# Performance work log

Measured on AMD Instinct MI355X. Metric: run time of the kernel, lower is better.

Reference implementation:

```python
import jax, jax.numpy as jnp
import numpy as np

D_MODEL = 1024
N_HEAD = 16
D_HEAD = D_MODEL // N_HEAD
D_FF = 4096
EPS = 1e-5


def _layernorm(x, gamma, beta):
    mu = jnp.mean(x, axis=-1, keepdims=True)
    var = jnp.mean(jnp.square(x - mu), axis=-1, keepdims=True)
    return (x - mu) * jax.lax.rsqrt(var + EPS) * gamma + beta


def setup_inputs() -> dict:
    key = jax.random.key(0)
    ks = jax.random.split(key, 16)
    s = 1.0 / np.sqrt(D_MODEL)
    sf = 1.0 / np.sqrt(D_FF)
    return {
        "src": jax.random.normal(ks[0], (8, 1024, D_MODEL), dtype=jnp.float32),
        "Wq": jax.random.uniform(ks[1], (D_MODEL, D_MODEL), jnp.float32, -s, s),
        "bq": jnp.zeros((D_MODEL,), jnp.float32),
        "Wk": jax.random.uniform(ks[2], (D_MODEL, D_MODEL), jnp.float32, -s, s),
        "bk": jnp.zeros((D_MODEL,), jnp.float32),
        "Wv": jax.random.uniform(ks[3], (D_MODEL, D_MODEL), jnp.float32, -s, s),
        "bv": jnp.zeros((D_MODEL,), jnp.float32),
        "Wo": jax.random.uniform(ks[4], (D_MODEL, D_MODEL), jnp.float32, -s, s),
        "bo": jnp.zeros((D_MODEL,), jnp.float32),
        "W1": jax.random.uniform(ks[5], (D_MODEL, D_FF), jnp.float32, -s, s),
        "b1": jnp.zeros((D_FF,), jnp.float32),
        "W2": jax.random.uniform(ks[6], (D_FF, D_MODEL), jnp.float32, -sf, sf),
        "b2": jnp.zeros((D_MODEL,), jnp.float32),
        "g1": jnp.ones((D_MODEL,), jnp.float32),
        "beta1": jnp.zeros((D_MODEL,), jnp.float32),
        "g2": jnp.ones((D_MODEL,), jnp.float32),
        "beta2": jnp.zeros((D_MODEL,), jnp.float32),
    }


def reference(src, Wq, bq, Wk, bk, Wv, bv, Wo, bo, W1, b1, W2, b2, g1, beta1, g2, beta2):
    B, S, _ = src.shape
    x = _layernorm(src, g1, beta1)
    # QKV projections -> [B, H, S, Dh]
    def split_heads(t):
        return t.reshape(B, S, N_HEAD, D_HEAD).transpose(0, 2, 1, 3)
    q = split_heads(x @ Wq + bq)
    k = split_heads(x @ Wk + bk)
    v = split_heads(x @ Wv + bv)
    # SymbolicAttention (canonical graph): softmax(q k^T / sqrt(d_head)) v
    scores = jnp.einsum('bhqd,bhkd->bhqk', q, k) / np.sqrt(D_HEAD).astype(np.float32)
    attn = jax.nn.softmax(scores, axis=-1)
    ctx = jnp.einsum('bhqk,bhkd->bhqd', attn, v)
    ctx = ctx.transpose(0, 2, 1, 3).reshape(B, S, D_MODEL)
    src = src + (ctx @ Wo + bo)  # dropout is identity in eval
    y = _layernorm(src, g2, beta2)
    ffn = jax.nn.relu(y @ W1 + b1) @ W2 + b2
    return src + ffn
```

## Files before the change

### kernel.cpp

```cpp
#include <hip/hip_runtime.h>
#include <stdint.h>

#define D_MODEL 1024
#define N_HEAD  16
#define D_HEAD  64
#define D_FF    4096
#define SEQ     1024
#define BATCH   8
#define M_TOK   (BATCH*SEQ)

typedef __attribute__((ext_vector_type(8))) short bf16x8;
typedef __attribute__((ext_vector_type(4))) float f32x4;

__device__ __forceinline__ float bf2f(unsigned short u) {
    union { unsigned int u; float f; } x; x.u = ((unsigned int)u) << 16; return x.f;
}
__device__ __forceinline__ unsigned short f2bf(float f) {
    union { float f; unsigned int u; } x; x.f = f;
    unsigned int r = x.u + 0x7fffu + ((x.u >> 16) & 1u);
    return (unsigned short)(r >> 16);
}

typedef const __attribute__((address_space(1))) unsigned int* gas_t;
typedef __attribute__((address_space(3))) unsigned int* las_t;
__device__ __forceinline__ void gl_lds16(const unsigned short* g, unsigned short* l) {
    __builtin_amdgcn_global_load_lds((gas_t)g, (las_t)l, 16, 0, 0);
}

__global__ __launch_bounds__(256) void transpose_cvt(
        const float* __restrict__ src, unsigned short* __restrict__ dst,
        int R, int C)
{
    __shared__ float t[32][33];
    const int tx = threadIdx.x & 31, ty = threadIdx.x >> 5;
    const int c0 = blockIdx.x * 32, r0 = blockIdx.y * 32;
    #pragma unroll
    for (int i = 0; i < 32; i += 8)
        t[ty + i][tx] = src[(size_t)(r0 + ty + i) * C + c0 + tx];
    __syncthreads();
    #pragma unroll
    for (int i = 0; i < 32; i += 8)
        dst[(size_t)(c0 + ty + i) * R + r0 + tx] = f2bf(t[tx][ty + i]);
}

__global__ __launch_bounds__(256) void ln_kernel(
        const float* __restrict__ x, const float* __restrict__ g,
        const float* __restrict__ be, unsigned short* __restrict__ out)
{
    const int row = blockIdx.x, tid = threadIdx.x;
    const f32x4 v = *(const f32x4*)(x + (size_t)row * D_MODEL + tid * 4);
    float s  = v[0] + v[1] + v[2] + v[3];
    float ss = v[0]*v[0] + v[1]*v[1] + v[2]*v[2] + v[3]*v[3];
    #pragma unroll
    for (int o = 1; o < 64; o <<= 1) { s += __shfl_xor(s, o); ss += __shfl_xor(ss, o); }
    __shared__ float sa[4], sb[4];
    const int wv = tid >> 6;
    if ((tid & 63) == 0) { sa[wv] = s; sb[wv] = ss; }
    __syncthreads();
    s  = sa[0] + sa[1] + sa[2] + sa[3];
    ss = sb[0] + sb[1] + sb[2] + sb[3];
    const float mu   = s * (1.0f / D_MODEL);
    const float rstd = rsqrtf(ss * (1.0f / D_MODEL) - mu * mu + 1e-5f);
    const f32x4 gv = *(const f32x4*)(g  + tid * 4);
    const f32x4 bv = *(const f32x4*)(be + tid * 4);
    unsigned short w[4];
    #pragma unroll
    for (int j = 0; j < 4; j++) w[j] = f2bf((v[j] - mu) * rstd * gv[j] + bv[j]);
    *(uint2*)(out + (size_t)row * D_MODEL + tid * 4) = *(uint2*)w;
}

template<bool OUT_BF16, bool RELU, bool RESID, bool VT_OUT>
__global__ __launch_bounds__(256) void gemm_bf16_tn(
        const unsigned short* __restrict__ A,
        const unsigned short* __restrict__ BT,
        const float* __restrict__ bias,
        const float* __restrict__ resid,
        void* __restrict__ Cout,
        int M, int N, int K, float scale)
{
    __shared__ unsigned short As[128 * 32];
    __shared__ unsigned short Bs[128 * 32];

    const int tid  = threadIdx.x;
    const int wave = tid >> 6, lane = tid & 63;
    const int quad = lane >> 4, l16 = lane & 15;
    const int m0 = blockIdx.y * 128, n0 = blockIdx.x * 128;
    const int wm = (wave >> 1) * 64, wn = (wave & 1) * 64;

    const int su_r = tid >> 2;
    const int su_k = (tid & 3) * 8;
    unsigned short* AsW = As + wave * 512;
    unsigned short* BsW = Bs + wave * 512;
    const unsigned short* gA0 = A  + (size_t)(m0 + su_r) * K + su_k;
    const unsigned short* gA1 = gA0 + (size_t)64 * K;
    const unsigned short* gB0 = BT + (size_t)(n0 + su_r) * K + su_k;
    const unsigned short* gB1 = gB0 + (size_t)64 * K;

    f32x4 acc[4][4] = {};

    for (int k0 = 0; k0 < K; k0 += 32) {
        __syncthreads();
        gl_lds16(gA0 + k0, AsW);
        gl_lds16(gA1 + k0, AsW + 2048);
        gl_lds16(gB0 + k0, BsW);
        gl_lds16(gB1 + k0, BsW + 2048);
        __syncthreads();

        bf16x8 af[4], bfr[4];
        #pragma unroll
        for (int mi = 0; mi < 4; mi++)
            af[mi] = *(const bf16x8*)(As + (wm + mi * 16 + l16) * 32 + quad * 8);
        #pragma unroll
        for (int ni = 0; ni < 4; ni++)
            bfr[ni] = *(const bf16x8*)(Bs + (wn + ni * 16 + l16) * 32 + quad * 8);
        #pragma unroll
        for (int mi = 0; mi < 4; mi++)
            #pragma unroll
            for (int ni = 0; ni < 4; ni++)
                acc[mi][ni] = __builtin_amdgcn_mfma_f32_16x16x32_bf16(
                        af[mi], bfr[ni], acc[mi][ni], 0, 0, 0);
    }

    #pragma unroll
    for (int mi = 0; mi < 4; mi++) {
        const int row_b = m0 + wm + mi * 16 + quad * 4;
        #pragma unroll
        for (int ni = 0; ni < 4; ni++) {
            const int col = n0 + wn + ni * 16 + l16;
            const float bsv = bias[col];
            if (VT_OUT) {
                const int bb = row_b >> 10, s = row_b & 1023;
                const int h = col >> 6, dd = col & 63;
                unsigned short w[4];
                #pragma unroll
                for (int r = 0; r < 4; r++)
                    w[r] = f2bf((acc[mi][ni][r] + bsv) * scale);
                *(uint2*)((unsigned short*)Cout
                          + ((size_t)((bb * 16 + h) * 64 + dd)) * 1024 + s) = *(uint2*)w;
            } else {
                #pragma unroll
                for (int r = 0; r < 4; r++) {
                    const int row = row_b + r;
                    float val = (acc[mi][ni][r] + bsv) * scale;
                    if (RELU)  val = fmaxf(val, 0.0f);
                    if (RESID) val += resid[(size_t)row * N + col];
                    if (OUT_BF16)
                        ((unsigned short*)Cout)[(size_t)row * N + col] = f2bf(val);
                    else
                        ((float*)Cout)[(size_t)row * N + col] = val;
                }
            }
        }
    }
}

#define ASTR 72
__global__ __launch_bounds__(256) void attn_mfma(
        const unsigned short* __restrict__ Q,
        const unsigned short* __restrict__ K,
        const unsigned short* __restrict__ VT,
        unsigned short* __restrict__ CTX)
{
    __shared__ unsigned short Ks[64 * ASTR];
    __shared__ unsigned short Vs[64 * ASTR];
    __shared__ unsigned short Ps[128 * ASTR];

    const int tid  = threadIdx.x;
    const int wave = tid >> 6, lane = tid & 63;
    const int quad = lane >> 4, l16 = lane & 15;
    const int bh = blockIdx.y;
    const int q0 = blockIdx.x * 128;
    const size_t baseQ = (size_t)(bh >> 4) * SEQ * D_MODEL + (size_t)(bh & 15) * D_HEAD;
    const size_t baseV = (size_t)bh * D_HEAD * SEQ;
    const int strip = wave * 32;

    bf16x8 qf[2][2];
    #pragma unroll
    for (int mt = 0; mt < 2; mt++)
        #pragma unroll
        for (int h = 0; h < 2; h++)
            qf[mt][h] = *(const bf16x8*)(Q + baseQ
                        + (size_t)(q0 + strip + mt * 16 + l16) * D_MODEL
                        + h * 32 + quad * 8);

    f32x4 of[2][4] = {};
    float l_p[2][4] = {};

    for (int c = 0; c < SEQ / 64; c++) {
        const int k0 = c * 64;
        __syncthreads();
        #pragma unroll
        for (int u = tid; u < 512; u += 256) {
            const int r = u >> 3, g = (u & 7) * 8;
            *(uint4*)(Ks + r * ASTR + g) =
                *(const uint4*)(K + baseQ + (size_t)(k0 + r) * D_MODEL + g);
            *(uint4*)(Vs + r * ASTR + g) =
                *(const uint4*)(VT + baseV + (size_t)r * SEQ + k0 + g);
        }
        __syncthreads();

        bf16x8 kf[4][2];
        #pragma unroll
        for (int kt = 0; kt < 4; kt++)
            #pragma unroll
            for (int h = 0; h < 2; h++)
                kf[kt][h] = *(const bf16x8*)(Ks + (kt * 16 + l16) * ASTR + h * 32 + quad * 8);

        #pragma unroll
        for (int mt = 0; mt < 2; mt++) {
            f32x4 s[4] = {};
            #pragma unroll
            for (int h = 0; h < 2; h++)
                #pragma unroll
                for (int kt = 0; kt < 4; kt++)
                    s[kt] = __builtin_amdgcn_mfma_f32_16x16x32_bf16(
                            qf[mt][h], kf[kt][h], s[kt], 0, 0, 0);
            #pragma unroll
            for (int kt = 0; kt < 4; kt++)
                #pragma unroll
                for (int r = 0; r < 4; r++) {
                    const float p = __expf(s[kt][r]);
                    l_p[mt][r] += p;
                    Ps[(strip + mt * 16 + quad * 4 + r) * ASTR + kt * 16 + l16] = f2bf(p);
                }
        }

        bf16x8 pf[2][2];
        #pragma unroll
        for (int mt = 0; mt < 2; mt++)
            #pragma unroll
            for (int h = 0; h < 2; h++)
                pf[mt][h] = *(const bf16x8*)(Ps + (strip + mt * 16 + l16) * ASTR
                                             + h * 32 + quad * 8);
        #pragma unroll
        for (int nt = 0; nt < 4; nt++) {
            bf16x8 vf[2];
            #pragma unroll
            for (int h = 0; h < 2; h++)
                vf[h] = *(const bf16x8*)(Vs + (nt * 16 + l16) * ASTR + h * 32 + quad * 8);
            #pragma unroll
            for (int mt = 0; mt < 2; mt++)
                #pragma unroll
                for (int h = 0; h < 2; h++)
                    of[mt][nt] = __builtin_amdgcn_mfma_f32_16x16x32_bf16(
                            pf[mt][h], vf[h], of[mt][nt], 0, 0, 0);
        }
    }

    #pragma unroll
    for (int mt = 0; mt < 2; mt++) {
        float inv[4];
        #pragma unroll
        for (int r = 0; r < 4; r++) {
            float l = l_p[mt][r];
            #pragma unroll
            for (int o = 1; o < 16; o <<= 1) l += __shfl_xor(l, o);
            inv[r] = 1.0f / l;
        }
        #pragma unroll
        for (int nt = 0; nt < 4; nt++)
            #pragma unroll
            for (int r = 0; r < 4; r++)
                CTX[baseQ + (size_t)(q0 + strip + mt * 16 + quad * 4 + r) * D_MODEL
                    + nt * 16 + l16] = f2bf(of[mt][nt][r] * inv[r]);
    }
}

extern "C" void kernel_launch(void* const* d_in, const int* in_sizes, int n_in,
                              void* d_out, int out_size, void* d_ws, size_t ws_size,
                              hipStream_t stream)
{
    (void)in_sizes; (void)n_in; (void)out_size; (void)ws_size;
    const float* src = (const float*)d_in[0];
    const float* Wq  = (const float*)d_in[1];
    const float* bq  = (const float*)d_in[2];
    const float* Wk  = (const float*)d_in[3];
    const float* bk  = (const float*)d_in[4];
    const float* Wv  = (const float*)d_in[5];
    const float* bv  = (const float*)d_in[6];
    const float* Wo  = (const float*)d_in[7];
    const float* bo  = (const float*)d_in[8];
    const float* W1  = (const float*)d_in[9];
    const float* b1  = (const float*)d_in[10];
    const float* W2  = (const float*)d_in[11];
    const float* b2  = (const float*)d_in[12];
    const float* g1  = (const float*)d_in[13];
    const float* be1 = (const float*)d_in[14];
    const float* g2  = (const float*)d_in[15];
    const float* be2 = (const float*)d_in[16];
    float* out = (float*)d_out;

    unsigned short* wqT = (unsigned short*)d_ws;
    unsigned short* wkT = wqT + 1024 * 1024;
    unsigned short* wvT = wkT + 1024 * 1024;
    unsigned short* woT = wvT + 1024 * 1024;
    unsigned short* w1T = woT + 1024 * 1024;
    unsigned short* w2T = w1T + 4096 * 1024;
    unsigned short* xn  = w2T + 1024 * 4096;
    unsigned short* q   = xn  + (size_t)M_TOK * D_MODEL;
    unsigned short* k   = q   + (size_t)M_TOK * D_MODEL;
    unsigned short* vT  = k   + (size_t)M_TOK * D_MODEL;
    unsigned short* ctx = vT  + (size_t)M_TOK * D_MODEL;
    unsigned short* hid = ctx + (size_t)M_TOK * D_MODEL;

    const dim3 blk(256);

    transpose_cvt<<<dim3(32, 32),  blk, 0, stream>>>(Wq, wqT, 1024, 1024);
    transpose_cvt<<<dim3(32, 32),  blk, 0, stream>>>(Wk, wkT, 1024, 1024);
    transpose_cvt<<<dim3(32, 32),  blk, 0, stream>>>(Wv, wvT, 1024, 1024);
    transpose_cvt<<<dim3(32, 32),  blk, 0, stream>>>(Wo, woT, 1024, 1024);
    transpose_cvt<<<dim3(128, 32), blk, 0, stream>>>(W1, w1T, 1024, 4096);
    transpose_cvt<<<dim3(32, 128), blk, 0, stream>>>(W2, w2T, 4096, 1024);

    ln_kernel<<<M_TOK, blk, 0, stream>>>(src, g1, be1, xn);

    gemm_bf16_tn<true,  false, false, false><<<dim3(8, 64), blk, 0, stream>>>(
        xn, wqT, bq, nullptr, q, M_TOK, D_MODEL, D_MODEL, 0.125f);
    gemm_bf16_tn<true,  false, false, false><<<dim3(8, 64), blk, 0, stream>>>(
        xn, wkT, bk, nullptr, k, M_TOK, D_MODEL, D_MODEL, 1.0f);
    gemm_bf16_tn<true,  false, false, true ><<<dim3(8, 64), blk, 0, stream>>>(
        xn, wvT, bv, nullptr, vT, M_TOK, D_MODEL, D_MODEL, 1.0f);

    attn_mfma<<<dim3(SEQ / 128, BATCH * N_HEAD), blk, 0, stream>>>(q, k, vT, ctx);

    gemm_bf16_tn<false, false, true,  false><<<dim3(8, 64), blk, 0, stream>>>(
        ctx, woT, bo, src, out, M_TOK, D_MODEL, D_MODEL, 1.0f);

    ln_kernel<<<M_TOK, blk, 0, stream>>>(out, g2, be2, xn);

    gemm_bf16_tn<true,  true,  false, false><<<dim3(32, 64), blk, 0, stream>>>(
        xn, w1T, b1, nullptr, hid, M_TOK, D_FF, D_MODEL, 1.0f);

    gemm_bf16_tn<false, false, true,  false><<<dim3(8, 64), blk, 0, stream>>>(
        hid, w2T, b2, out, out, M_TOK, D_MODEL, D_FF, 1.0f);
}
```

Baseline: 566.4 us.

## Fuse QKV projections into one GEMM and use K=64 swizzled LDS tiles

Stores the Q, K and V weights transposed side by side so a single GEMM launch with N=3072 produces all three projections. Its epilogue routes columns to the q, k and transposed v buffers with the right bias and scale. The GEMM k-step doubles to 64 with an XOR-swizzled LDS layout. This halves the number of barrier-separated load phases and is meant to avoid LDS bank conflicts on the fragment reads. The cost is double the shared memory per block, which may lower occupancy, plus extra branching in the epilogue.

```diff
diff --git a/kernel.cpp b/kernel.cpp
--- a/kernel.cpp
+++ b/kernel.cpp
@@ -69,17 +69,19 @@
     *(uint2*)(out + (size_t)row * D_MODEL + tid * 4) = *(uint2*)w;
 }
 
-template<bool OUT_BF16, bool RELU, bool RESID, bool VT_OUT>
+template<int MODE>
 __global__ __launch_bounds__(256) void gemm_bf16_tn(
         const unsigned short* __restrict__ A,
         const unsigned short* __restrict__ BT,
         const float* __restrict__ bias,
+        const float* __restrict__ bias2,
+        const float* __restrict__ bias3,
         const float* __restrict__ resid,
         void* __restrict__ Cout,
-        int M, int N, int K, float scale)
-{
-    __shared__ unsigned short As[128 * 32];
-    __shared__ unsigned short Bs[128 * 32];
+        int M, int N, int K)
+{
+    __shared__ unsigned short As[128 * 64];
+    __shared__ unsigned short Bs[128 * 64];
 
     const int tid  = threadIdx.x;
     const int wave = tid >> 6, lane = tid & 63;
@@ -87,38 +89,43 @@
     const int m0 = blockIdx.y * 128, n0 = blockIdx.x * 128;
     const int wm = (wave >> 1) * 64, wn = (wave & 1) * 64;
 
-    const int su_r = tid >> 2;
-    const int su_k = (tid & 3) * 8;
-    unsigned short* AsW = As + wave * 512;
-    unsigned short* BsW = Bs + wave * 512;
-    const unsigned short* gA0 = A  + (size_t)(m0 + su_r) * K + su_k;
-    const unsigned short* gA1 = gA0 + (size_t)64 * K;
-    const unsigned short* gB0 = BT + (size_t)(n0 + su_r) * K + su_k;
-    const unsigned short* gB1 = gB0 + (size_t)64 * K;
+    const int st_row = wave * 8 + ((tid >> 3) & 7);
+    const int st_g   = (tid & 7) ^ ((tid >> 3) & 7);
+    const unsigned short* gA = A  + (size_t)(m0 + st_row) * K + st_g * 8;
+    const unsigned short* gB = BT + (size_t)(n0 + st_row) * K + st_g * 8;
+    unsigned short* lA = As + wave * 512;
+    unsigned short* lB = Bs + wave * 512;
+    const int rx = l16 & 7;
 
     f32x4 acc[4][4] = {};
 
-    for (int k0 = 0; k0 < K; k0 += 32) {
+    for (int k0 = 0; k0 < K; k0 += 64) {
         __syncthreads();
-        gl_lds16(gA0 + k0, AsW);
-        gl_lds16(gA1 + k0, AsW + 2048);
-        gl_lds16(gB0 + k0, BsW);
-        gl_lds16(gB1 + k0, BsW + 2048);
+        #pragma unroll
+        for (int j = 0; j < 4; j++) {
+            gl_lds16(gA + (size_t)j * 32 * K + k0, lA + j * 2048);
+            gl_lds16(gB + (size_t)j * 32 * K + k0, lB + j * 2048);
+        }
         __syncthreads();
 
-        bf16x8 af[4], bfr[4];
-        #pragma unroll
-        for (int mi = 0; mi < 4; mi++)
-            af[mi] = *(const bf16x8*)(As + (wm + mi * 16 + l16) * 32 + quad * 8);
-        #pragma unroll
-        for (int ni = 0; ni < 4; ni++)
-            bfr[ni] = *(const bf16x8*)(Bs + (wn + ni * 16 + l16) * 32 + quad * 8);
-        #pragma unroll
-        for (int mi = 0; mi < 4; mi++)
+        #pragma unroll
+        for (int h = 0; h < 2; h++) {
+            bf16x8 af[4], bfr[4];
+            #pragma unroll
+            for (int mi = 0; mi < 4; mi++)
+                af[mi] = *(const bf16x8*)(As + (wm + mi * 16 + l16) * 64
+                                          + ((h * 4 + quad) ^ rx) * 8);
             #pragma unroll
             for (int ni = 0; ni < 4; ni++)
-                acc[mi][ni] = __builtin_amdgcn_mfma_f32_16x16x32_bf16(
-                        af[mi], bfr[ni], acc[mi][ni], 0, 0, 0);
+                bfr[ni] = *(const bf16x8*)(Bs + (wn + ni * 16 + l16) * 64
+                                           + ((h * 4 + quad) ^ rx) * 8);
+            #pragma unroll
+            for (int mi = 0; mi < 4; mi++)
+                #pragma unroll
+                for (int ni = 0; ni < 4; ni++)
+                    acc[mi][ni] = __builtin_amdgcn_mfma_f32_16x16x32_bf16(
+                            af[mi], bfr[ni], acc[mi][ni], 0, 0, 0);
+        }
     }
 
     #pragma unroll
@@ -127,27 +134,41 @@
         #pragma unroll
         for (int ni = 0; ni < 4; ni++) {
             const int col = n0 + wn + ni * 16 + l16;
-            const float bsv = bias[col];
-            if (VT_OUT) {
-                const int bb = row_b >> 10, s = row_b & 1023;
-                const int h = col >> 6, dd = col & 63;
-                unsigned short w[4];
+            if (MODE == 1) {
+                const float bsv = bias[col];
                 #pragma unroll
                 for (int r = 0; r < 4; r++)
-                    w[r] = f2bf((acc[mi][ni][r] + bsv) * scale);
-                *(uint2*)((unsigned short*)Cout
-                          + ((size_t)((bb * 16 + h) * 64 + dd)) * 1024 + s) = *(uint2*)w;
+                    ((unsigned short*)Cout)[(size_t)(row_b + r) * N + col] =
+                        f2bf(fmaxf(acc[mi][ni][r] + bsv, 0.0f));
+            } else if (MODE == 2) {
+                const float bsv = bias[col];
+                #pragma unroll
+                for (int r = 0; r < 4; r++)
+                    ((float*)Cout)[(size_t)(row_b + r) * N + col] =
+                        acc[mi][ni][r] + bsv +
+                        resid[(size_t)(row_b + r) * N + col];
             } else {
-                #pragma unroll
-                for (int r = 0; r < 4; r++) {
-                    const int row = row_b + r;
-                    float val = (acc[mi][ni][r] + bsv) * scale;
-                    if (RELU)  val = fmaxf(val, 0.0f);
-                    if (RESID) val += resid[(size_t)row * N + col];
-                    if (OUT_BF16)
-                        ((unsigned short*)Cout)[(size_t)row * N + col] = f2bf(val);
-                    else
-                        ((float*)Cout)[(size_t)row * N + col] = val;
+                if (col < 2048) {
+                    const float sc  = (col < 1024) ? 0.125f : 1.0f;
+                    const float bsv = (col < 1024) ? bias[col] : bias2[col - 1024];
+                    unsigned short* dst = (unsigned short*)Cout
+                        + (size_t)(col >> 10) * M_TOK * 1024;
+                    #pragma unroll
+                    for (int r = 0; r < 4; r++)
+                        dst[(size_t)(row_b + r) * 1024 + (col & 1023)] =
+                            f2bf((acc[mi][ni][r] + bsv) * sc);
+                } else {
+                    const int cc = col - 2048;
+                    const float bsv = bias3[cc];
+                    const int bb = row_b >> 10, s = row_b & 1023;
+                    const int h = cc >> 6, dd = cc & 63;
+                    unsigned short w[4];
+                    #pragma unroll
+                    for (int r = 0; r < 4; r++)
+                        w[r] = f2bf(acc[mi][ni][r] + bsv);
+                    *(uint2*)((unsigned short*)Cout + (size_t)2 * M_TOK * 1024
+                              + ((size_t)((bb * 16 + h) * 64 + dd)) * 1024 + s)
+                        = *(uint2*)w;
                 }
             }
         }
@@ -290,13 +311,11 @@
     const float* be2 = (const float*)d_in[16];
     float* out = (float*)d_out;
 
-    unsigned short* wqT = (unsigned short*)d_ws;
-    unsigned short* wkT = wqT + 1024 * 1024;
-    unsigned short* wvT = wkT + 1024 * 1024;
-    unsigned short* woT = wvT + 1024 * 1024;
+    unsigned short* wqkvT = (unsigned short*)d_ws;
+    unsigned short* woT = wqkvT + (size_t)3 * 1024 * 1024;
     unsigned short* w1T = woT + 1024 * 1024;
-    unsigned short* w2T = w1T + 4096 * 1024;
-    unsigned short* xn  = w2T + 1024 * 4096;
+    unsigned short* w2T = w1T + (size_t)4096 * 1024;
+    unsigned short* xn  = w2T + (size_t)1024 * 4096;
     unsigned short* q   = xn  + (size_t)M_TOK * D_MODEL;
     unsigned short* k   = q   + (size_t)M_TOK * D_MODEL;
     unsigned short* vT  = k   + (size_t)M_TOK * D_MODEL;
@@ -305,32 +324,28 @@
 
     const dim3 blk(256);
 
-    transpose_cvt<<<dim3(32, 32),  blk, 0, stream>>>(Wq, wqT, 1024, 1024);
-    transpose_cvt<<<dim3(32, 32),  blk, 0, stream>>>(Wk, wkT, 1024, 1024);
-    transpose_cvt<<<dim3(32, 32),  blk, 0, stream>>>(Wv, wvT, 1024, 1024);
+    transpose_cvt<<<dim3(32, 32),  blk, 0, stream>>>(Wq, wqkvT,                 1024, 1024);
+    transpose_cvt<<<dim3(32, 32),  blk, 0, stream>>>(Wk, wqkvT + 1024 * 1024,   1024, 1024);
+    transpose_cvt<<<dim3(32, 32),  blk, 0, stream>>>(Wv, wqkvT + 2 * 1024 * 1024, 1024, 1024);
     transpose_cvt<<<dim3(32, 32),  blk, 0, stream>>>(Wo, woT, 1024, 1024);
     transpose_cvt<<<dim3(128, 32), blk, 0, stream>>>(W1, w1T, 1024, 4096);
     transpose_cvt<<<dim3(32, 128), blk, 0, stream>>>(W2, w2T, 4096, 1024);
 
     ln_kernel<<<M_TOK, blk, 0, stream>>>(src, g1, be1, xn);
 
-    gemm_bf16_tn<true,  false, false, false><<<dim3(8, 64), blk, 0, stream>>>(
-        xn, wqT, bq, nullptr, q, M_TOK, D_MODEL, D_MODEL, 0.125f);
-    gemm_bf16_tn<true,  false, false, false><<<dim3(8, 64), blk, 0, stream>>>(
-        xn, wkT, bk, nullptr, k, M_TOK, D_MODEL, D_MODEL, 1.0f);
-    gemm_bf16_tn<true,  false, false, true ><<<dim3(8, 64), blk, 0, stream>>>(
-        xn, wvT, bv, nullptr, vT, M_TOK, D_MODEL, D_MODEL, 1.0f);
+    gemm_bf16_tn<3><<<dim3(24, 64), blk, 0, stream>>>(
+        xn, wqkvT, bq, bk, bv, nullptr, q, M_TOK, 3072, D_MODEL);
 
     attn_mfma<<<dim3(SEQ / 128, BATCH * N_HEAD), blk, 0, stream>>>(q, k, vT, ctx);
 
-    gemm_bf16_tn<false, false, true,  false><<<dim3(8, 64), blk, 0, stream>>>(
-        ctx, woT, bo, src, out, M_TOK, D_MODEL, D_MODEL, 1.0f);
+    gemm_bf16_tn<2><<<dim3(8, 64), blk, 0, stream>>>(
+        ctx, woT, bo, nullptr, nullptr, src, out, M_TOK, D_MODEL, D_MODEL);
 
     ln_kernel<<<M_TOK, blk, 0, stream>>>(out, g2, be2, xn);
 
-    gemm_bf16_tn<true,  true,  false, false><<<dim3(32, 64), blk, 0, stream>>>(
-        xn, w1T, b1, nullptr, hid, M_TOK, D_FF, D_MODEL, 1.0f);
-
-    gemm_bf16_tn<false, false, true,  false><<<dim3(8, 64), blk, 0, stream>>>(
-        hid, w2T, b2, out, out, M_TOK, D_MODEL, D_FF, 1.0f);
-}
+    gemm_bf16_tn<1><<<dim3(32, 64), blk, 0, stream>>>(
+        xn, w1T, b1, nullptr, nullptr, nullptr, hid, M_TOK, D_FF, D_MODEL);
+
+    gemm_bf16_tn<2><<<dim3(8, 64), blk, 0, stream>>>(
+        hid, w2T, b2, nullptr, nullptr, out, out, M_TOK, D_MODEL, D_FF);
+}
```

Result: faster. 503.9 us (-11.0%).
